# Optimization experiments

Measured on AMD Instinct MI355X. Metric: run time of the kernel, lower is better.

Reference implementation:

```python
import jax, jax.numpy as jnp
import numpy as np

TEMPERATURE = 0.07
BASE_TEMPERATURE = 0.07


def setup_inputs() -> dict:
    key = jax.random.key(0)
    k1, k2 = jax.random.split(key)
    feat1 = jax.random.normal(k1, (4096, 128), dtype=jnp.float32)
    feat2 = jax.random.normal(k2, (4096, 128), dtype=jnp.float32)
    return {"feat1": feat1, "feat2": feat2}


def reference(feat1, feat2):
    # world_size = 1 -> gather is identity; N = per-gpu batch size
    N = feat1.shape[0]
    two_n = 2 * N
    features = jnp.concatenate([feat1, feat2], axis=0)          # [2N, C]
    # F.normalize(dim=1)
    norm = jnp.linalg.norm(features, axis=1, keepdims=True)
    features = features / jnp.maximum(norm, 1e-12)
    logits = jnp.matmul(features, features.T) / TEMPERATURE      # [2N, 2N]
    logits = logits - jax.lax.stop_gradient(
        jnp.max(logits, axis=1, keepdims=True))
    # neg_mask = ~eye: sum of exp over off-diagonal entries per row
    exp_sum = jnp.sum(jnp.exp(logits), axis=1) - jnp.exp(jnp.diagonal(logits))
    # pos_mask: row i pairs with column (i + N) mod 2N
    idx = jnp.arange(two_n)
    pos = logits[idx, (idx + N) % two_n]                          # [2N]
    log_prob = pos - jnp.log(exp_sum)
    loss = -(TEMPERATURE / BASE_TEMPERATURE) * jnp.mean(log_prob)
    return loss
```

## Files before the change

### kernel.cpp

```cpp
#include <hip/hip_runtime.h>

typedef unsigned short u16;
typedef __attribute__((ext_vector_type(8))) short short8;
typedef __attribute__((ext_vector_type(4))) float f32x4;

#define INVT 14.285714285714286f

__device__ __forceinline__ u16 f2bf(float f) {
  union { float f; unsigned u; } v; v.f = f;
  unsigned u = v.u;
  u += 0x7fffu + ((u >> 16) & 1u);
  return (u16)(u >> 16);
}
__device__ __forceinline__ float bf2f(u16 h) {
  union { unsigned u; float f; } v; v.u = ((unsigned)h) << 16;
  return v.f;
}

__global__ void norm_kernel(const float* __restrict__ f1, const float* __restrict__ f2,
                            u16* __restrict__ F, float* __restrict__ dvec,
                            float* __restrict__ pos, float* __restrict__ E, int N) {
  int i = blockIdx.x;
  int l = threadIdx.x;
  if (l < 2) E[2 * i + l] = 0.0f;
  const float* a = f1 + (size_t)i * 128;
  const float* b = f2 + (size_t)i * 128;
  float a0 = a[l], a1 = a[l + 64];
  float b0 = b[l], b1 = b[l + 64];
  float sa = a0 * a0 + a1 * a1;
  float sb = b0 * b0 + b1 * b1;
#pragma unroll
  for (int o = 32; o; o >>= 1) { sa += __shfl_xor(sa, o); sb += __shfl_xor(sb, o); }
  float ia = 1.0f / fmaxf(sqrtf(sa), 1e-12f);
  float ib = 1.0f / fmaxf(sqrtf(sb), 1e-12f);
  u16 ba0 = f2bf(a0 * ia), ba1 = f2bf(a1 * ia);
  u16 bb0 = f2bf(b0 * ib), bb1 = f2bf(b1 * ib);
  u16* Fa = F + (size_t)i * 128;
  u16* Fb = F + (size_t)(i + N) * 128;
  Fa[l] = ba0; Fa[l + 64] = ba1;
  Fb[l] = bb0; Fb[l + 64] = bb1;
  float fa0 = bf2f(ba0), fa1 = bf2f(ba1);
  float fb0 = bf2f(bb0), fb1 = bf2f(bb1);
  float s1 = fa0 * fa0 + fa1 * fa1;
  float s2 = fb0 * fb0 + fb1 * fb1;
  float cr = fa0 * fb0 + fa1 * fb1;
#pragma unroll
  for (int o = 32; o; o >>= 1) {
    s1 += __shfl_xor(s1, o); s2 += __shfl_xor(s2, o); cr += __shfl_xor(cr, o);
  }
  if (l == 0) {
    dvec[i]     = __expf((s1 - 1.0f) * INVT);
    dvec[i + N] = __expf((s2 - 1.0f) * INVT);
    pos[i] = cr;
    pos[i + N] = cr;
  }
}

__device__ __forceinline__ void glds16(const u16* g, u16* l) {
  __builtin_amdgcn_global_load_lds((const __attribute__((address_space(1))) void*)g,
                                   (__attribute__((address_space(3))) void*)l,
                                   16, 0, 0);
}

__global__ __launch_bounds__(256, 2) void gemm_exp_kernel(const u16* __restrict__ F,
                                                          float* __restrict__ E) {
  __shared__ __align__(16) u16 At[128 * 128];
  __shared__ __align__(16) u16 Bt[128 * 128];
  __shared__ float colsum[128];
  __shared__ float rowsum[128];
  const int tid = threadIdx.x;
  const int wave = tid >> 6, lane = tid & 63;
  int p = blockIdx.x;
  int r = (int)((sqrtf(8.0f * (float)p + 1.0f) - 1.0f) * 0.5f);
  while ((r + 1) * (r + 2) / 2 <= p) ++r;
  while (r * (r + 1) / 2 > p) --r;
  const int bj = r, bi = p - r * (r + 1) / 2;
  const u16* Ab = F + (size_t)bi * (128 * 128);
  const u16* Bb = F + (size_t)bj * (128 * 128);
  if (tid < 128) { colsum[tid] = 0.0f; rowsum[tid] = 0.0f; }
#pragma unroll
  for (int t = 0; t < 8; ++t) {
    int chunk = wave * 8 + t;
    int g = chunk * 64 + lane;
    int gg = g ^ ((g >> 4) & 7);
    glds16(Ab + (size_t)gg * 8, &At[chunk * 512]);
    glds16(Bb + (size_t)gg * 8, &Bt[chunk * 512]);
  }
  __syncthreads();

  const int wr = wave >> 1, wc = wave & 1;
  const int q = lane >> 4, m = lane & 15;
  f32x4 acc[4][4];
#pragma unroll
  for (int fr = 0; fr < 4; ++fr)
#pragma unroll
    for (int cf = 0; cf < 4; ++cf) acc[fr][cf] = (f32x4)(0.0f);

#pragma unroll
  for (int ks = 0; ks < 4; ++ks) {
    const int c = ks * 4 + q;
    short8 av[4], bv[4];
#pragma unroll
    for (int fr = 0; fr < 4; ++fr) {
      int rr = wr * 64 + fr * 16 + m;
      av[fr] = *(const short8*)&At[rr * 128 + ((c ^ (rr & 7)) * 8)];
    }
#pragma unroll
    for (int cf = 0; cf < 4; ++cf) {
      int rr = wc * 64 + cf * 16 + m;
      bv[cf] = *(const short8*)&Bt[rr * 128 + ((c ^ (rr & 7)) * 8)];
    }
#pragma unroll
    for (int fr = 0; fr < 4; ++fr)
#pragma unroll
      for (int cf = 0; cf < 4; ++cf)
        acc[fr][cf] = __builtin_amdgcn_mfma_f32_16x16x32_bf16(av[fr], bv[cf], acc[fr][cf], 0, 0, 0);
  }

  float cs[4] = {0.f, 0.f, 0.f, 0.f};
  float rs[16];
#pragma unroll
  for (int i = 0; i < 16; ++i) rs[i] = 0.f;
#pragma unroll
  for (int cf = 0; cf < 4; ++cf)
#pragma unroll
    for (int fr = 0; fr < 4; ++fr)
#pragma unroll
      for (int rg = 0; rg < 4; ++rg) {
        float e = __expf((acc[fr][cf][rg] - 1.0f) * INVT);
        cs[cf] += e;
        rs[fr * 4 + rg] += e;
      }
#pragma unroll
  for (int cf = 0; cf < 4; ++cf) {
    cs[cf] += __shfl_xor(cs[cf], 16);
    cs[cf] += __shfl_xor(cs[cf], 32);
    if (q == 0) atomicAdd(&colsum[wc * 64 + cf * 16 + m], cs[cf]);
  }
  if (bi != bj) {
#pragma unroll
    for (int i = 0; i < 16; ++i) {
#pragma unroll
      for (int o = 1; o < 16; o <<= 1) rs[i] += __shfl_xor(rs[i], o);
    }
    if (m == 0) {
#pragma unroll
      for (int i = 0; i < 16; ++i)
        atomicAdd(&rowsum[wr * 64 + (i >> 2) * 16 + q * 4 + (i & 3)], rs[i]);
    }
  }
  __syncthreads();
  if (tid < 128) {
    atomicAdd(&E[bj * 128 + tid], colsum[tid]);
    if (bi != bj) atomicAdd(&E[bi * 128 + tid], rowsum[tid]);
  }
}

__global__ void finish_kernel(const float* __restrict__ E, const float* __restrict__ dvec,
                              const float* __restrict__ pos, float* __restrict__ out,
                              int TWO_N, float scale) {
  float t = 0.0f;
  for (int i = threadIdx.x; i < TWO_N; i += 1024)
    t += (pos[i] - 1.0f) * INVT - logf(E[i] - dvec[i]);
#pragma unroll
  for (int o = 32; o; o >>= 1) t += __shfl_xor(t, o);
  __shared__ float wsum[16];
  int wave = threadIdx.x >> 6, lane = threadIdx.x & 63;
  if (lane == 0) wsum[wave] = t;
  __syncthreads();
  if (threadIdx.x == 0) {
    float s = 0.0f;
#pragma unroll
    for (int k = 0; k < 16; ++k) s += wsum[k];
    out[0] = s * scale;
  }
}

extern "C" void kernel_launch(void* const* d_in, const int* in_sizes, int n_in,
                              void* d_out, int out_size, void* d_ws, size_t ws_size,
                              hipStream_t stream) {
  const float* f1 = (const float*)d_in[0];
  const float* f2 = (const float*)d_in[1];
  const int N = in_sizes[0] / 128;
  const int TWO_N = 2 * N;
  const int NB = TWO_N / 128;
  const int NTILES = NB * (NB + 1) / 2;

  char* ws = (char*)d_ws;
  u16*   F    = (u16*)ws;
  float* dvec = (float*)(ws + (size_t)TWO_N * 128 * 2);
  float* pos  = dvec + TWO_N;
  float* E    = pos + TWO_N;

  norm_kernel<<<N, 64, 0, stream>>>(f1, f2, F, dvec, pos, E, N);
  gemm_exp_kernel<<<NTILES, 256, 0, stream>>>(F, E);
  finish_kernel<<<1, 1024, 0, stream>>>(E, dvec, pos, (float*)d_out, TWO_N,
                                        -1.0f / (float)TWO_N);
}
```

Measured before the change: 89.35 us.

## Persistent tile loop with B reuse, fused finish via last-block ticket

The GEMM kernel becomes persistent with 512 blocks, each walking a contiguous range of lower-triangular tiles. It reloads the B tile only when the column block changes and reuses B as A on diagonal tiles. The finish kernel is folded into the GEMM through an atomic ticket so the last block computes the loss. The norm kernel packs 8 rows per 256-thread block, exp is rewritten as exp2 with an FMA, and the row-sum reduction uses a transpose-style shuffle tree with one atomic per lane. The aim is to cut launch overhead, redundant global-to-LDS loads and shuffle count, at the cost of less parallel slack and a serial tail in the last block.

```diff
diff --git a/kernel.cpp b/kernel.cpp
--- a/kernel.cpp
+++ b/kernel.cpp
@@ -5,6 +5,7 @@
 typedef __attribute__((ext_vector_type(4))) float f32x4;
 
 #define INVT 14.285714285714286f
+#define KEXP 20.617062471830945f
 
 __device__ __forceinline__ u16 f2bf(float f) {
   union { float f; unsigned u; } v; v.f = f;
@@ -16,163 +17,202 @@
   union { unsigned u; float f; } v; v.u = ((unsigned)h) << 16;
   return v.f;
 }
-
-__global__ void norm_kernel(const float* __restrict__ f1, const float* __restrict__ f2,
-                            u16* __restrict__ F, float* __restrict__ dvec,
-                            float* __restrict__ pos, float* __restrict__ E, int N) {
-  int i = blockIdx.x;
-  int l = threadIdx.x;
-  if (l < 2) E[2 * i + l] = 0.0f;
-  const float* a = f1 + (size_t)i * 128;
-  const float* b = f2 + (size_t)i * 128;
-  float a0 = a[l], a1 = a[l + 64];
-  float b0 = b[l], b1 = b[l + 64];
-  float sa = a0 * a0 + a1 * a1;
-  float sb = b0 * b0 + b1 * b1;
-#pragma unroll
-  for (int o = 32; o; o >>= 1) { sa += __shfl_xor(sa, o); sb += __shfl_xor(sb, o); }
-  float ia = 1.0f / fmaxf(sqrtf(sa), 1e-12f);
-  float ib = 1.0f / fmaxf(sqrtf(sb), 1e-12f);
-  u16 ba0 = f2bf(a0 * ia), ba1 = f2bf(a1 * ia);
-  u16 bb0 = f2bf(b0 * ib), bb1 = f2bf(b1 * ib);
-  u16* Fa = F + (size_t)i * 128;
-  u16* Fb = F + (size_t)(i + N) * 128;
-  Fa[l] = ba0; Fa[l + 64] = ba1;
-  Fb[l] = bb0; Fb[l + 64] = bb1;
-  float fa0 = bf2f(ba0), fa1 = bf2f(ba1);
-  float fb0 = bf2f(bb0), fb1 = bf2f(bb1);
-  float s1 = fa0 * fa0 + fa1 * fa1;
-  float s2 = fb0 * fb0 + fb1 * fb1;
-  float cr = fa0 * fb0 + fa1 * fb1;
-#pragma unroll
-  for (int o = 32; o; o >>= 1) {
-    s1 += __shfl_xor(s1, o); s2 += __shfl_xor(s2, o); cr += __shfl_xor(cr, o);
-  }
-  if (l == 0) {
-    dvec[i]     = __expf((s1 - 1.0f) * INVT);
-    dvec[i + N] = __expf((s2 - 1.0f) * INVT);
-    pos[i] = cr;
-    pos[i + N] = cr;
-  }
-}
-
 __device__ __forceinline__ void glds16(const u16* g, u16* l) {
   __builtin_amdgcn_global_load_lds((const __attribute__((address_space(1))) void*)g,
                                    (__attribute__((address_space(3))) void*)l,
                                    16, 0, 0);
 }
 
-__global__ __launch_bounds__(256, 2) void gemm_exp_kernel(const u16* __restrict__ F,
-                                                          float* __restrict__ E) {
+__global__ __launch_bounds__(256) void norm_kernel(
+    const float* __restrict__ f1, const float* __restrict__ f2,
+    u16* __restrict__ F, float* __restrict__ dvec, float* __restrict__ pos,
+    float* __restrict__ E, int* __restrict__ done, int N) {
+  const int b = blockIdx.x, tid = threadIdx.x;
+  const int wave = tid >> 6, l = tid & 63;
+  int gid = b * 256 + tid;
+  if (gid < 2 * N) E[gid] = 0.0f;
+  if (gid == 0) *done = 0;
+#pragma unroll
+  for (int it = 0; it < 2; ++it) {
+    int i = b * 8 + wave * 2 + it;
+    if (i >= N) break;
+    const float* a = f1 + (size_t)i * 128;
+    const float* c = f2 + (size_t)i * 128;
+    float a0 = a[l], a1 = a[l + 64];
+    float b0 = c[l], b1 = c[l + 64];
+    float sa = a0 * a0 + a1 * a1;
+    float sb = b0 * b0 + b1 * b1;
+#pragma unroll
+    for (int o = 32; o; o >>= 1) { sa += __shfl_xor(sa, o); sb += __shfl_xor(sb, o); }
+    float ia = 1.0f / fmaxf(sqrtf(sa), 1e-12f);
+    float ib = 1.0f / fmaxf(sqrtf(sb), 1e-12f);
+    u16 ba0 = f2bf(a0 * ia), ba1 = f2bf(a1 * ia);
+    u16 bb0 = f2bf(b0 * ib), bb1 = f2bf(b1 * ib);
+    u16* Fa = F + (size_t)i * 128;
+    u16* Fb = F + (size_t)(i + N) * 128;
+    Fa[l] = ba0; Fa[l + 64] = ba1;
+    Fb[l] = bb0; Fb[l + 64] = bb1;
+    float fa0 = bf2f(ba0), fa1 = bf2f(ba1);
+    float fb0 = bf2f(bb0), fb1 = bf2f(bb1);
+    float s1 = fa0 * fa0 + fa1 * fa1;
+    float s2 = fb0 * fb0 + fb1 * fb1;
+    float cr = fa0 * fb0 + fa1 * fb1;
+#pragma unroll
+    for (int o = 32; o; o >>= 1) {
+      s1 += __shfl_xor(s1, o); s2 += __shfl_xor(s2, o); cr += __shfl_xor(cr, o);
+    }
+    if (l == 0) {
+      dvec[i]     = exp2f(fmaf(s1, KEXP, -KEXP));
+      dvec[i + N] = exp2f(fmaf(s2, KEXP, -KEXP));
+      pos[i] = cr;
+      pos[i + N] = cr;
+    }
+  }
+}
+
+__global__ __launch_bounds__(256, 2) void gemm_exp_kernel(
+    const u16* __restrict__ F, float* __restrict__ E,
+    const float* __restrict__ dvec, const float* __restrict__ pos,
+    int* __restrict__ done, float* __restrict__ out, int TWO_N, int NT) {
   __shared__ __align__(16) u16 At[128 * 128];
   __shared__ __align__(16) u16 Bt[128 * 128];
   __shared__ float colsum[128];
   __shared__ float rowsum[128];
-  const int tid = threadIdx.x;
+  __shared__ int ticket_s;
+  const int b = blockIdx.x, tid = threadIdx.x;
   const int wave = tid >> 6, lane = tid & 63;
-  int p = blockIdx.x;
-  int r = (int)((sqrtf(8.0f * (float)p + 1.0f) - 1.0f) * 0.5f);
-  while ((r + 1) * (r + 2) / 2 <= p) ++r;
-  while (r * (r + 1) / 2 > p) --r;
-  const int bj = r, bi = p - r * (r + 1) / 2;
-  const u16* Ab = F + (size_t)bi * (128 * 128);
-  const u16* Bb = F + (size_t)bj * (128 * 128);
-  if (tid < 128) { colsum[tid] = 0.0f; rowsum[tid] = 0.0f; }
-#pragma unroll
-  for (int t = 0; t < 8; ++t) {
-    int chunk = wave * 8 + t;
-    int g = chunk * 64 + lane;
-    int gg = g ^ ((g >> 4) & 7);
-    glds16(Ab + (size_t)gg * 8, &At[chunk * 512]);
-    glds16(Bb + (size_t)gg * 8, &Bt[chunk * 512]);
-  }
-  __syncthreads();
-
+  const int G = gridDim.x;
+
+  const int start = (int)(((long)NT * b) / G);
+  const int end   = (int)(((long)NT * (b + 1)) / G);
+  int bj = (int)((sqrtf(8.0f * (float)start + 1.0f) - 1.0f) * 0.5f);
+  while ((bj + 1) * (bj + 2) / 2 <= start) ++bj;
+  while (bj * (bj + 1) / 2 > start) --bj;
+  int bi = start - bj * (bj + 1) / 2;
+  int cur_bj = -1;
   const int wr = wave >> 1, wc = wave & 1;
   const int q = lane >> 4, m = lane & 15;
-  f32x4 acc[4][4];
-#pragma unroll
-  for (int fr = 0; fr < 4; ++fr)
-#pragma unroll
-    for (int cf = 0; cf < 4; ++cf) acc[fr][cf] = (f32x4)(0.0f);
-
-#pragma unroll
-  for (int ks = 0; ks < 4; ++ks) {
-    const int c = ks * 4 + q;
-    short8 av[4], bv[4];
-#pragma unroll
-    for (int fr = 0; fr < 4; ++fr) {
-      int rr = wr * 64 + fr * 16 + m;
-      av[fr] = *(const short8*)&At[rr * 128 + ((c ^ (rr & 7)) * 8)];
-    }
+
+  for (int p = start; p < end; ++p) {
+    if (tid < 128) { colsum[tid] = 0.0f; rowsum[tid] = 0.0f; }
+    const bool diag = (bi == bj);
+    if (bj != cur_bj) {
+      const u16* Bb = F + (size_t)bj * (128 * 128);
+#pragma unroll
+      for (int t = 0; t < 8; ++t) {
+        int chunk = wave * 8 + t;
+        int g = chunk * 64 + lane;
+        int gg = g ^ ((g >> 4) & 7);
+        glds16(Bb + (size_t)gg * 8, &Bt[chunk * 512]);
+      }
+      cur_bj = bj;
+    }
+    if (!diag) {
+      const u16* Ab = F + (size_t)bi * (128 * 128);
+#pragma unroll
+      for (int t = 0; t < 8; ++t) {
+        int chunk = wave * 8 + t;
+        int g = chunk * 64 + lane;
+        int gg = g ^ ((g >> 4) & 7);
+        glds16(Ab + (size_t)gg * 8, &At[chunk * 512]);
+      }
+    }
+    __syncthreads();
+
+    const u16* asrc = diag ? Bt : At;
+    f32x4 acc[4][4];
+#pragma unroll
+    for (int fr = 0; fr < 4; ++fr)
+#pragma unroll
+      for (int cf = 0; cf < 4; ++cf) acc[fr][cf] = (f32x4)(0.0f);
+
+#pragma unroll
+    for (int ks = 0; ks < 4; ++ks) {
+      const int c = ks * 4 + q;
+      short8 av[4], bv[4];
+#pragma unroll
+      for (int fr = 0; fr < 4; ++fr) {
+        int rr = wr * 64 + fr * 16 + m;
+        av[fr] = *(const short8*)&asrc[rr * 128 + ((c ^ (rr & 7)) * 8)];
+      }
+#pragma unroll
+      for (int cf = 0; cf < 4; ++cf) {
+        int rr = wc * 64 + cf * 16 + m;
+        bv[cf] = *(const short8*)&Bt[rr * 128 + ((c ^ (rr & 7)) * 8)];
+      }
+#pragma unroll
+      for (int fr = 0; fr < 4; ++fr)
+#pragma unroll
+        for (int cf = 0; cf < 4; ++cf)
+          acc[fr][cf] = __builtin_amdgcn_mfma_f32_16x16x32_bf16(av[fr], bv[cf], acc[fr][cf], 0, 0, 0);
+    }
+
+    float cs[4] = {0.f, 0.f, 0.f, 0.f};
+    float v[16];
+#pragma unroll
+    for (int i = 0; i < 16; ++i) v[i] = 0.f;
+#pragma unroll
+    for (int cf = 0; cf < 4; ++cf)
+#pragma unroll
+      for (int fr = 0; fr < 4; ++fr)
+#pragma unroll
+        for (int rg = 0; rg < 4; ++rg) {
+          float e = exp2f(fmaf(acc[fr][cf][rg], KEXP, -KEXP));
+          cs[cf] += e;
+          v[fr * 4 + rg] += e;
+        }
 #pragma unroll
     for (int cf = 0; cf < 4; ++cf) {
-      int rr = wc * 64 + cf * 16 + m;
-      bv[cf] = *(const short8*)&Bt[rr * 128 + ((c ^ (rr & 7)) * 8)];
-    }
-#pragma unroll
-    for (int fr = 0; fr < 4; ++fr)
-#pragma unroll
-      for (int cf = 0; cf < 4; ++cf)
-        acc[fr][cf] = __builtin_amdgcn_mfma_f32_16x16x32_bf16(av[fr], bv[cf], acc[fr][cf], 0, 0, 0);
+      cs[cf] += __shfl_xor(cs[cf], 16);
+      cs[cf] += __shfl_xor(cs[cf], 32);
+      if (q == 0) atomicAdd(&colsum[wc * 64 + cf * 16 + m], cs[cf]);
+    }
+    if (!diag) {
+      float t16[16];
+#pragma unroll
+      for (int i = 0; i < 16; ++i) t16[i] = __shfl_xor(v[i], 8);
+      bool hi = (m & 8) != 0;
+#pragma unroll
+      for (int i = 0; i < 8; ++i) v[i] = hi ? (v[i + 8] + t16[i + 8]) : (v[i] + t16[i]);
+#pragma unroll
+      for (int i = 0; i < 8; ++i) t16[i] = __shfl_xor(v[i], 4);
+      hi = (m & 4) != 0;
+#pragma unroll
+      for (int i = 0; i < 4; ++i) v[i] = hi ? (v[i + 4] + t16[i + 4]) : (v[i] + t16[i]);
+#pragma unroll
+      for (int i = 0; i < 4; ++i) t16[i] = __shfl_xor(v[i], 2);
+      hi = (m & 2) != 0;
+#pragma unroll
+      for (int i = 0; i < 2; ++i) v[i] = hi ? (v[i + 2] + t16[i + 2]) : (v[i] + t16[i]);
+      t16[0] = __shfl_xor(v[0], 1);
+      t16[1] = __shfl_xor(v[1], 1);
+      v[0] = (m & 1) ? (v[1] + t16[1]) : (v[0] + t16[0]);
+      atomicAdd(&rowsum[wr * 64 + (m >> 2) * 16 + q * 4 + (m & 3)], v[0]);
+    }
+    __syncthreads();
+    if (tid < 128) {
+      atomicAdd(&E[bj * 128 + tid], colsum[tid]);
+      if (!diag) atomicAdd(&E[bi * 128 + tid], rowsum[tid]);
+    }
+    ++bi;
+    if (bi > bj) { bi = 0; ++bj; }
   }
 
-  float cs[4] = {0.f, 0.f, 0.f, 0.f};
-  float rs[16];
-#pragma unroll
-  for (int i = 0; i < 16; ++i) rs[i] = 0.f;
-#pragma unroll
-  for (int cf = 0; cf < 4; ++cf)
-#pragma unroll
-    for (int fr = 0; fr < 4; ++fr)
-#pragma unroll
-      for (int rg = 0; rg < 4; ++rg) {
-        float e = __expf((acc[fr][cf][rg] - 1.0f) * INVT);
-        cs[cf] += e;
-        rs[fr * 4 + rg] += e;
-      }
-#pragma unroll
-  for (int cf = 0; cf < 4; ++cf) {
-    cs[cf] += __shfl_xor(cs[cf], 16);
-    cs[cf] += __shfl_xor(cs[cf], 32);
-    if (q == 0) atomicAdd(&colsum[wc * 64 + cf * 16 + m], cs[cf]);
-  }
-  if (bi != bj) {
-#pragma unroll
-    for (int i = 0; i < 16; ++i) {
-#pragma unroll
-      for (int o = 1; o < 16; o <<= 1) rs[i] += __shfl_xor(rs[i], o);
-    }
-    if (m == 0) {
-#pragma unroll
-      for (int i = 0; i < 16; ++i)
-        atomicAdd(&rowsum[wr * 64 + (i >> 2) * 16 + q * 4 + (i & 3)], rs[i]);
-    }
-  }
+  __threadfence();
+  if (tid == 0) ticket_s = atomicAdd(done, 1);
   __syncthreads();
-  if (tid < 128) {
-    atomicAdd(&E[bj * 128 + tid], colsum[tid]);
-    if (bi != bj) atomicAdd(&E[bi * 128 + tid], rowsum[tid]);
-  }
-}
-
-__global__ void finish_kernel(const float* __restrict__ E, const float* __restrict__ dvec,
-                              const float* __restrict__ pos, float* __restrict__ out,
-                              int TWO_N, float scale) {
-  float t = 0.0f;
-  for (int i = threadIdx.x; i < TWO_N; i += 1024)
-    t += (pos[i] - 1.0f) * INVT - logf(E[i] - dvec[i]);
-#pragma unroll
-  for (int o = 32; o; o >>= 1) t += __shfl_xor(t, o);
-  __shared__ float wsum[16];
-  int wave = threadIdx.x >> 6, lane = threadIdx.x & 63;
-  if (lane == 0) wsum[wave] = t;
-  __syncthreads();
-  if (threadIdx.x == 0) {
-    float s = 0.0f;
-#pragma unroll
-    for (int k = 0; k < 16; ++k) s += wsum[k];
-    out[0] = s * scale;
+  if (ticket_s == G - 1) {
+    float t = 0.0f;
+    for (int i = tid; i < TWO_N; i += 256) {
+      float e = atomicAdd(&E[i], 0.0f);
+      t += (pos[i] - 1.0f) * INVT - logf(e - dvec[i]);
+    }
+#pragma unroll
+    for (int o = 32; o; o >>= 1) t += __shfl_xor(t, o);
+    if (lane == 0) colsum[wave] = t;
+    __syncthreads();
+    if (tid == 0)
+      out[0] = (colsum[0] + colsum[1] + colsum[2] + colsum[3]) * (-1.0f / (float)TWO_N);
   }
 }
 
@@ -181,19 +221,19 @@
                               hipStream_t stream) {
   const float* f1 = (const float*)d_in[0];
   const float* f2 = (const float*)d_in[1];
-  const int N = in_sizes[0] / 128;
-  const int TWO_N = 2 * N;
-  const int NB = TWO_N / 128;
-  const int NTILES = NB * (NB + 1) / 2;
+  int N = in_sizes[0] / 128;
+  int TWO_N = 2 * N;
+  int NB = TWO_N / 128;
+  int NT = NB * (NB + 1) / 2;
 
   char* ws = (char*)d_ws;
   u16*   F    = (u16*)ws;
   float* dvec = (float*)(ws + (size_t)TWO_N * 128 * 2);
   float* pos  = dvec + TWO_N;
   float* E    = pos + TWO_N;
-
-  norm_kernel<<<N, 64, 0, stream>>>(f1, f2, F, dvec, pos, E, N);
-  gemm_exp_kernel<<<NTILES, 256, 0, stream>>>(F, E);
-  finish_kernel<<<1, 1024, 0, stream>>>(E, dvec, pos, (float*)d_out, TWO_N,
-                                        -1.0f / (float)TWO_N);
-}
+  int*   done = (int*)(E + TWO_N);
+
+  norm_kernel<<<512, 256, 0, stream>>>(f1, f2, F, dvec, pos, E, done, N);
+  gemm_exp_kernel<<<512, 256, 0, stream>>>(F, E, dvec, pos, done, (float*)d_out,
+                                           TWO_N, NT);
+}
```

Result: slower. 120.8 us (+35.2%).
